# Kernel tuning notes

Measured on AMD Instinct MI355X. Metric: run time of the kernel, lower is better.

## Reference

```python
import jax, jax.numpy as jnp
import numpy as np

EPS = 1e-5

def _ln(x, g, b):
    mu = x.mean(-1, keepdims=True)
    v = x.var(-1, keepdims=True)
    return g * (x - mu) / jnp.sqrt(v + EPS) + b

def _mlp(x, W0, b0, g0, be0, W1, b1, g1, be1, W2, b2, nm):
    # Linear -> LN -> GELU, Linear -> LN -> GELU, Linear -> split into complex
    h = jax.nn.gelu(_ln(x @ W0 + b0, g0, be0), approximate=False)
    h = jax.nn.gelu(_ln(h @ W1 + b1, g1, be1), approximate=False)
    o = h @ W2 + b2
    return jax.lax.complex(o[..., :nm], o[..., nm:])

def _forward(x, w_W0, w_b0, w_g0, w_be0, w_W1, w_b1, w_g1, w_be1, w_W2, w_b2,
             h_W0, h_b0, h_g0, h_be0, h_W1, h_b1, h_g1, h_be1, h_W2, h_b2,
             freq_r, freq_i, mixer_w, mixer_b, norm_g, norm_b, sc_w, sc_b):
    B, C, H, W = x.shape
    m1, m2 = freq_r.shape[2], freq_r.shape[3]
    wc = jnp.linspace(0.0, 1.0, W, dtype=x.dtype)
    hc = jnp.linspace(0.0, 1.0, H, dtype=x.dtype)
    # W-basis conditioned on values and normalized w-coordinate
    x_nhwc = x.transpose(0, 2, 3, 1)                                   # (B,H,W,C)
    w_in = jnp.concatenate([x_nhwc, jnp.broadcast_to(wc[None, None, :, None], (B, H, W, 1))], -1)
    wb = _mlp(w_in, w_W0, w_b0, w_g0, w_be0, w_W1, w_b1, w_g1, w_be1, w_W2, w_b2, m2)  # (B,H,W,m2) c64
    xc = x.astype(jnp.complex64)
    t = jnp.einsum('bchw,bhwm->bchm', xc, wb)                          # (B,C,H,m2)
    # H-basis conditioned on real part of W-transformed signal
    h_in = jnp.concatenate([t.real.transpose(0, 3, 2, 1),
                            jnp.broadcast_to(hc[None, None, :, None], (B, m2, H, 1))], -1)
    hb = _mlp(h_in, h_W0, h_b0, h_g0, h_be0, h_W1, h_b1, h_g1, h_be1, h_W2, h_b2, m1)  # (B,m2,H,m1)
    t2 = jnp.einsum('bchm,bmhn->bcnm', t, hb)                          # (B,C,m1,m2)
    Wf = jax.lax.complex(freq_r, freq_i)                               # (C,O,m1,m2)
    proc = jnp.einsum('bixy,oixy->boxy', t2, Wf)                       # (B,O,m1,m2)
    # Inverse transforms via conjugate-transposed bases
    rec_h = jnp.einsum('bonm,bmhn->bohm', proc, jnp.conj(hb))          # (B,O,H,m2)
    rec = jnp.einsum('bohm,bhwm->bohw', rec_h, jnp.conj(wb))           # (B,O,H,W)
    y = rec.real / (H * W)
    y = jnp.einsum('bchw,oc->bohw', y, mixer_w) + mixer_b[None, :, None, None]
    mu = y.mean(1, keepdims=True)
    v = y.var(1, keepdims=True)
    y = norm_g[None, :, None, None] * (y - mu) / jnp.sqrt(v + EPS) + norm_b[None, :, None, None]
    y = jax.nn.gelu(y, approximate=False)
    sc = jnp.einsum('bchw,oc->bohw', x, sc_w) + sc_b[None, :, None, None]
    return jax.nn.gelu(y + sc, approximate=False)

def setup_inputs() -> dict:
    key = jax.random.key(0)
    B, C, O, H, W, M1, M2, HD = 8, 64, 64, 192, 192, 48, 48, 64
    ks = jax.random.split(key, 12)
    r = lambda k, sh, s=0.05: jax.random.normal(k, sh, jnp.float32) * s
    d = dict(x=jax.random.normal(ks[0], (B, C, H, W), jnp.float32))
    d.update(w_W0=r(ks[1], (C + 1, HD)), w_b0=jnp.zeros(HD), w_g0=jnp.ones(HD), w_be0=jnp.zeros(HD),
             w_W1=r(ks[2], (HD, HD)), w_b1=jnp.zeros(HD), w_g1=jnp.ones(HD), w_be1=jnp.zeros(HD),
             w_W2=r(ks[3], (HD, 2 * M2)), w_b2=jnp.zeros(2 * M2))
    d.update(h_W0=r(ks[4], (C + 1, HD)), h_b0=jnp.zeros(HD), h_g0=jnp.ones(HD), h_be0=jnp.zeros(HD),
             h_W1=r(ks[5], (HD, HD)), h_b1=jnp.zeros(HD), h_g1=jnp.ones(HD), h_be1=jnp.zeros(HD),
             h_W2=r(ks[6], (HD, 2 * M1)), h_b2=jnp.zeros(2 * M1))
    d.update(freq_r=r(ks[7], (C, O, M1, M2), 0.1), freq_i=r(ks[8], (C, O, M1, M2), 0.1),
             mixer_w=r(ks[9], (O, O)), mixer_b=jnp.zeros(O),
             norm_g=jnp.ones(O), norm_b=jnp.zeros(O),
             sc_w=r(ks[10], (O, C)), sc_b=jnp.zeros(O))
    return d

def reference(x, w_W0, w_b0, w_g0, w_be0, w_W1, w_b1, w_g1, w_be1, w_W2, w_b2,
              h_W0, h_b0, h_g0, h_be0, h_W1, h_b1, h_g1, h_be1, h_W2, h_b2,
              freq_r, freq_i, mixer_w, mixer_b, norm_g, norm_b, sc_w, sc_b):
    return _forward(x, w_W0, w_b0, w_g0, w_be0, w_W1, w_b1, w_g1, w_be1, w_W2, w_b2,
                    h_W0, h_b0, h_g0, h_be0, h_W1, h_b1, h_g1, h_be1, h_W2, h_b2,
                    freq_r, freq_i, mixer_w, mixer_b, norm_g, norm_b, sc_w, sc_b)
```

## Files before the change

### kernel.cpp

```cpp
#include <hip/hip_runtime.h>
#include <math.h>

#define LN_EPS 1e-5f

typedef short bf16x8 __attribute__((ext_vector_type(8)));
typedef float f32x4  __attribute__((ext_vector_type(4)));

__device__ __forceinline__ float gelu_f(float v) {
    return 0.5f * v * (1.0f + erff(v * 0.70710678118654752f));
}
__device__ __forceinline__ unsigned short f2bf(float f) {
    __bf16 h = (__bf16)f;
    unsigned short u;
    __builtin_memcpy(&u, &h, 2);
    return u;
}
__device__ __forceinline__ float bf2f(unsigned short h) {
    return __uint_as_float(((unsigned)h) << 16);
}

__global__ __launch_bounds__(256) void k0_swizzle(
    const float* __restrict__ wW0, const float* __restrict__ wW1, const float* __restrict__ wW2,
    const float* __restrict__ hW0, const float* __restrict__ hW1, const float* __restrict__ hW2,
    uint4* __restrict__ dst)
// ... 205 lines not shown
    for (int cc = 0; cc < 16; ++cc) {
        int c = cc*4 + quad;
        float v = x[((b*64 + c)*192 + h)*192 + (w0 + r)];
        unsigned short hv = f2bf(v);
        aHi[r*72 + c] = hv;
        aLo[r*72 + c] = f2bf(v - bf2f(hv));
    }
    mlp_body(aHi, aLo, wsw, W0full + 64*64, b0, g0, be0, b1, g1, be1, b2,
             (float)w0, wb_r, wb_i, bh*192 + w0);
}

__global__ __launch_bounds__(256) void k3_mlp_h(
    const float* __restrict__ t_r, const float* __restrict__ W0full,
    const float* __restrict__ b0, const float* __restrict__ g0, const float* __restrict__ be0,
    const float* __restrict__ b1, const float* __restrict__ g1, const float* __restrict__ be1,
    const float* __restrict__ b2,
    const uint4* __restrict__ wsw,
    float* __restrict__ hb_r, float* __restrict__ hb_i)
{
    __shared__ unsigned short aHi[64*72];
    __shared__ unsigned short aLo[64*72];
    int tid = threadIdx.x;
    int wv = __builtin_amdgcn_readfirstlane(tid >> 6);
    int lane = tid & 63, li = lane & 15, quad = lane >> 4;
    int hq = blockIdx.x % 3;
    int bm = blockIdx.x / 3;
    int b = bm / 48, m = bm % 48;
    int h0 = hq * 64;
    int r = wv*16 + li;
    {
        const float4* tb = (const float4*)(t_r + ((b*48 + m)*192 + h0 + r)*64);
        #pragma unroll
        for (int q = 0; q < 4; ++q) {
            float4 v4 = tb[quad*4 + q];
            float vv[4] = {v4.x, v4.y, v4.z, v4.w};
            int k0 = quad*16 + q*4;
            #pragma unroll
            for (int e = 0; e < 4; ++e) {
                unsigned short hv = f2bf(vv[e]);
                aHi[r*72 + k0 + e] = hv;
                aLo[r*72 + k0 + e] = f2bf(vv[e] - bf2f(hv));
            }
        }
    }
    mlp_body(aHi, aLo, wsw, W0full + 64*64, b0, g0, be0, b1, g1, be1, b2,
             (float)h0, hb_r, hb_i, bm*192 + h0);
}

__global__ __launch_bounds__(256) void k2_t(
    const float* __restrict__ x,
    const float* __restrict__ wb_r, const float* __restrict__ wb_i,
    float* __restrict__ t_r, float* __restrict__ t_i)
{
    __shared__ unsigned short aHi[64*72];
    __shared__ unsigned short aLo[64*72];
    __shared__ uint4 bfrag[1536];
    float* cbuf = (float*)bfrag;
    int bh = blockIdx.x;
    int b = bh / 192, h = bh % 192;
    int tid = threadIdx.x;
    int wv = __builtin_amdgcn_readfirstlane(tid >> 6);
    int lane = tid & 63, li = lane & 15, quad = lane >> 4;
    int rbase = wv*16;
    int row = rbase + li;

    f32x4 acc[6];
    {
        f32x4 z = {0.f, 0.f, 0.f, 0.f};
        #pragma unroll
        for (int nt = 0; nt < 6; ++nt) acc[nt] = z;
    }
    union U { uint4 u; bf16x8 b8; };

    for (int w0 = 0; w0 < 192; w0 += 64) {
        if (w0) __syncthreads();
        {
            const float4* srow = (const float4*)(x + ((b*64 + row)*192 + h)*192 + w0) + quad*4;
            #pragma unroll
            for (int q = 0; q < 4; ++q) {
                float4 v4 = srow[q];
                float vv[4] = {v4.x, v4.y, v4.z, v4.w};
                int k0 = quad*16 + q*4;
                #pragma unroll
                for (int e = 0; e < 4; ++e) {
                    unsigned short hv = f2bf(vv[e]);
                    aHi[row*72 + k0 + e] = hv;
                    aLo[row*72 + k0 + e] = f2bf(vv[e] - bf2f(hv));
                }
            }
        }
        for (int t = tid >> 6; t < 12; t += 4) {
            int nt = t >> 1, ks = t & 1;
            const float* src = (nt < 3) ? wb_r : wb_i;
            int col = (nt < 3 ? nt : nt - 3)*16 + li;
            const float* sp = src + (bh*192 + w0 + ks*32 + quad*8)*48 + col;
            unsigned hi8[8], lo8[8];
            #pragma unroll
            for (int j = 0; j < 8; ++j) {
                float v = sp[j*48];
                unsigned short hv = f2bf(v);
                hi8[j] = hv;
                lo8[j] = f2bf(v - bf2f(hv));
            }
            uint4 ph, pl;
            ph.x = hi8[0] | (hi8[1]<<16); ph.y = hi8[2] | (hi8[3]<<16);
            ph.z = hi8[4] | (hi8[5]<<16); ph.w = hi8[6] | (hi8[7]<<16);
            pl.x = lo8[0] | (lo8[1]<<16); pl.y = lo8[2] | (lo8[3]<<16);
            pl.z = lo8[4] | (lo8[5]<<16); pl.w = lo8[6] | (lo8[7]<<16);
            bfrag[t*64 + lane]       = ph;
            bfrag[768 + t*64 + lane] = pl;
        }
        __syncthreads();
        bf16x8 aH[2], aL[2];
        #pragma unroll
        for (int ks = 0; ks < 2; ++ks) {
            aH[ks] = *(const bf16x8*)&aHi[row*72 + ks*32 + quad*8];
            aL[ks] = *(const bf16x8*)&aLo[row*72 + ks*32 + quad*8];
        }
        #pragma unroll
        for (int nt = 0; nt < 6; ++nt) {
            f32x4 a = acc[nt];
            #pragma unroll
            for (int ks = 0; ks < 2; ++ks) {
                int t = nt*2 + ks;
                U bh_, bl_;
                bh_.u = bfrag[t*64 + lane];
                bl_.u = bfrag[768 + t*64 + lane];
                a = __builtin_amdgcn_mfma_f32_16x16x32_bf16(aH[ks], bh_.b8, a, 0, 0, 0);
                a = __builtin_amdgcn_mfma_f32_16x16x32_bf16(aH[ks], bl_.b8, a, 0, 0, 0);
                a = __builtin_amdgcn_mfma_f32_16x16x32_bf16(aL[ks], bh_.b8, a, 0, 0, 0);
            }
            acc[nt] = a;
        }
    }
    __syncthreads();
    #pragma unroll
    for (int nt = 0; nt < 3; ++nt) {
        int m = nt*16 + li;
        #pragma unroll
        for (int rg = 0; rg < 4; ++rg) {
            int c = rbase + quad*4 + rg;
            cbuf[m*67 + c] = acc[nt][rg];
        }
    }
    __syncthreads();
    for (int idx = tid; idx < 3072; idx += 256) {
        int m = idx >> 6, c = idx & 63;
        t_r[((b*48 + m)*192 + h)*64 + c] = cbuf[m*67 + c];
    }
    __syncthreads();
    #pragma unroll
    for (int nt = 3; nt < 6; ++nt) {
        int m = (nt - 3)*16 + li;
        #pragma unroll
        for (int rg = 0; rg < 4; ++rg) {
            int c = rbase + quad*4 + rg;
            cbuf[m*67 + c] = acc[nt][rg];
        }
    }
    __syncthreads();
    for (int idx = tid; idx < 3072; idx += 256) {
        int m = idx >> 6, c = idx & 63;
        t_i[((b*48 + m)*192 + h)*64 + c] = cbuf[m*67 + c];
    }
}

__global__ __launch_bounds__(256) void k4_t2(
    const float* __restrict__ t_r, const float* __restrict__ t_i,
    const float* __restrict__ hb_r, const float* __restrict__ hb_i,
    float* __restrict__ t2_r, float* __restrict__ t2_i)
{
    __shared__ unsigned short aHi[64*72];
    __shared__ unsigned short aLo[64*72];
    __shared__ uint4 bfrag[1536];
    int bm = blockIdx.x;
    int b = bm / 48, m = bm % 48;
    int tid = threadIdx.x;
    int wv = __builtin_amdgcn_readfirstlane(tid >> 6);
    int lane = tid & 63, li = lane & 15, quad = lane >> 4;
    int rbase = wv*16;
    int row = rbase + li;

    f32x4 acc[6];
    {
        f32x4 z = {0.f, 0.f, 0.f, 0.f};
// ... 31 lines not shown
            }
            const float* sp = src + (bm*192 + h0 + ks*32 + quad*8)*48 + col;
            unsigned hi8[8], lo8[8];
            #pragma unroll
            for (int j = 0; j < 8; ++j) {
                float v = sgn * sp[j*48];
                unsigned short hv = f2bf(v);
                hi8[j] = hv;
                lo8[j] = f2bf(v - bf2f(hv));
            }
            uint4 ph, pl;
            ph.x = hi8[0] | (hi8[1]<<16); ph.y = hi8[2] | (hi8[3]<<16);
            ph.z = hi8[4] | (hi8[5]<<16); ph.w = hi8[6] | (hi8[7]<<16);
            pl.x = lo8[0] | (lo8[1]<<16); pl.y = lo8[2] | (lo8[3]<<16);
            pl.z = lo8[4] | (lo8[5]<<16); pl.w = lo8[6] | (lo8[7]<<16);
            bfrag[t*64 + lane]       = ph;
            bfrag[768 + t*64 + lane] = pl;
        }
        __syncthreads();
        bf16x8 aH[2], aL[2];
        #pragma unroll
        for (int ks = 0; ks < 2; ++ks) {
            aH[ks] = *(const bf16x8*)&aHi[row*72 + ks*32 + quad*8];
            aL[ks] = *(const bf16x8*)&aLo[row*72 + ks*32 + quad*8];
        }
        #pragma unroll
        for (int nt = 0; nt < 6; ++nt) {
            f32x4 a = acc[nt];
            #pragma unroll
            for (int ks = 0; ks < 2; ++ks) {
                int t = nt*2 + ks;
                U bh_, bl_;
                bh_.u = bfrag[t*64 + lane];
                bl_.u = bfrag[768 + t*64 + lane];
                a = __builtin_amdgcn_mfma_f32_16x16x32_bf16(aH[ks], bh_.b8, a, 0, 0, 0);
                a = __builtin_amdgcn_mfma_f32_16x16x32_bf16(aH[ks], bl_.b8, a, 0, 0, 0);
                a = __builtin_amdgcn_mfma_f32_16x16x32_bf16(aL[ks], bh_.b8, a, 0, 0, 0);
            }
            acc[nt] = a;
        }
    }
    #pragma unroll
    for (int nt = 0; nt < 6; ++nt) {
        #pragma unroll
        for (int rg = 0; rg < 4; ++rg) {
            int c = rbase + quad*4 + rg;
            float v = acc[nt][rg];
            if (nt < 3) t2_r[((b*64 + c)*48 + nt*16 + li)*48 + m]       = v;
            else        t2_i[((b*64 + c)*48 + (nt - 3)*16 + li)*48 + m] = v;
        }
    }
}

__global__ __launch_bounds__(256) void k5_proc(
    const float* __restrict__ t2_r, const float* __restrict__ t2_i,
    const float* __restrict__ fr, const float* __restrict__ fi,
    float* __restrict__ proc_r, float* __restrict__ proc_i)
{
    int og = blockIdx.x & 31;
    int ch = blockIdx.x >> 5;
    int nm = ch*256 + threadIdx.x;
    int n = nm / 48, mm = nm % 48;
    int o0 = og*2;
    float p0r[8], p0i[8], p1r[8], p1i[8];
    #pragma unroll
    for (int bb = 0; bb < 8; ++bb) { p0r[bb]=0.f; p0i[bb]=0.f; p1r[bb]=0.f; p1i[bb]=0.f; }
    for (int i = 0; i < 64; ++i) {
        float w0r = fr[(o0*64 + i)*2304 + nm];
        float w0i = fi[(o0*64 + i)*2304 + nm];
        float w1r = fr[((o0+1)*64 + i)*2304 + nm];
        float w1i = fi[((o0+1)*64 + i)*2304 + nm];
        #pragma unroll
        for (int bb = 0; bb < 8; ++bb) {
            float tr = t2_r[(bb*64 + i)*2304 + nm];
            float ti = t2_i[(bb*64 + i)*2304 + nm];
            p0r[bb] = fmaf(tr, w0r, fmaf(-ti, w0i, p0r[bb]));
            p0i[bb] = fmaf(tr, w0i, fmaf( ti, w0r, p0i[bb]));
            p1r[bb] = fmaf(tr, w1r, fmaf(-ti, w1i, p1r[bb]));
            p1i[bb] = fmaf(tr, w1i, fmaf( ti, w1r, p1i[bb]));
        }
    }
    #pragma unroll
    for (int bb = 0; bb < 8; ++bb) {
        int base0 = ((bb*48 + mm)*64 + o0)*48 + n;
        proc_r[base0]      = p0r[bb];
        proc_i[base0]      = p0i[bb];
        proc_r[base0 + 48] = p1r[bb];
        proc_i[base0 + 48] = p1i[bb];
    }
}

__global__ __launch_bounds__(256) void k6_rech(
    const float* __restrict__ proc_r, const float* __restrict__ proc_i,
    const float* __restrict__ hb_r, const float* __restrict__ hb_i,
    float* __restrict__ rh_r, float* __restrict__ rh_i)
{
    __shared__ unsigned short aHi[64*104];
    __shared__ unsigned short aLo[64*104];
    __shared__ uint4 bfrag[1536];
    int hq = blockIdx.x % 3;
    int bm = blockIdx.x / 3;
    int b = bm / 48, m = bm % 48;
    int h0 = hq * 64;
    int tid = threadIdx.x;
    int wv = __builtin_amdgcn_readfirstlane(tid >> 6);
    int lane = tid & 63, li = lane & 15, quad = lane >> 4;
    int rbase = wv*16;
    int row = rbase + li;

    {
        int hr = bm*192 + h0 + row;
        const float4* pr = (const float4*)(hb_r + hr*48) + quad*3;
        const float4* pi = (const float4*)(hb_i + hr*48) + quad*3;
        #pragma unroll
        for (int q = 0; q < 3; ++q) {
            float4 vr = pr[q];
            float4 vi = pi[q];
            int k0 = quad*12 + q*4;
            float vs[8] = {vr.x, vr.y, vr.z, vr.w, vi.x, vi.y, vi.z, vi.w};
            #pragma unroll
            for (int e = 0; e < 4; ++e) {
                unsigned short h1 = f2bf(vs[e]);
                aHi[row*104 + k0 + e] = h1;
                aLo[row*104 + k0 + e] = f2bf(vs[e] - bf2f(h1));
                unsigned short h2 = f2bf(vs[4+e]);
                aHi[row*104 + 48 + k0 + e] = h2;
                aLo[row*104 + 48 + k0 + e] = f2bf(vs[4+e] - bf2f(h2));
            }
        }
    }
    union U { uint4 u; bf16x8 b8; };
    bf16x8 aH[3], aL[3];
    #pragma unroll
    for (int ks = 0; ks < 3; ++ks) {
        aH[ks] = *(const bf16x8*)&aHi[row*104 + ks*32 + quad*8];
        aL[ks] = *(const bf16x8*)&aLo[row*104 + ks*32 + quad*8];
    }

    f32x4 accR[4], accI[4];
    for (int pass = 0; pass < 2; ++pass) {
        if (pass) __syncthreads();
        for (int t = tid >> 6; t < 12; t += 4) {
            int ks = t % 3;
            int nt = t / 3;
            int o = nt*16 + li;
            int kk0 = ks*32 + quad*8;
            const float* srcp;
            int n0;
            float sgn;
            if (kk0 < 48) { srcp = pass ? proc_i : proc_r; n0 = kk0;      sgn = 1.f; }
            else          { srcp = pass ? proc_r : proc_i; n0 = kk0 - 48; sgn = pass ? -1.f : 1.f; }
            const float* sp = srcp + ((b*48 + m)*64 + o)*48 + n0;
            float4 f0 = *(const float4*)sp;
            float4 f1 = *(const float4*)(sp + 4);
            float vv[8] = {f0.x, f0.y, f0.z, f0.w, f1.x, f1.y, f1.z, f1.w};
            unsigned hi8[8], lo8[8];
            #pragma unroll
            for (int j = 0; j < 8; ++j) {
                float v = sgn * vv[j];
                unsigned short hv = f2bf(v);
                hi8[j] = hv;
                lo8[j] = f2bf(v - bf2f(hv));
            }
            uint4 ph, pl;
            ph.x = hi8[0] | (hi8[1]<<16); ph.y = hi8[2] | (hi8[3]<<16);
            ph.z = hi8[4] | (hi8[5]<<16); ph.w = hi8[6] | (hi8[7]<<16);
            pl.x = lo8[0] | (lo8[1]<<16); pl.y = lo8[2] | (lo8[3]<<16);
            pl.z = lo8[4] | (lo8[5]<<16); pl.w = lo8[6] | (lo8[7]<<16);
            bfrag[t*64 + lane]       = ph;
            bfrag[768 + t*64 + lane] = pl;
        }
        __syncthreads();
        f32x4* acc = pass ? accI : accR;
        #pragma unroll
        for (int nt = 0; nt < 4; ++nt) {
            f32x4 a = {0.f, 0.f, 0.f, 0.f};
            #pragma unroll
            for (int ks = 0; ks < 3; ++ks) {
                int t = nt*3 + ks;
                U bh_, bl_;
                bh_.u = bfrag[t*64 + lane];
                bl_.u = bfrag[768 + t*64 + lane];
                a = __builtin_amdgcn_mfma_f32_16x16x32_bf16(aH[ks], bh_.b8, a, 0, 0, 0);
                a = __builtin_amdgcn_mfma_f32_16x16x32_bf16(aH[ks], bl_.b8, a, 0, 0, 0);
                a = __builtin_amdgcn_mfma_f32_16x16x32_bf16(aL[ks], bh_.b8, a, 0, 0, 0);
            }
            acc[nt] = a;
        }
    }
    #pragma unroll
    for (int nt = 0; nt < 4; ++nt) {
        int o = nt*16 + li;
        #pragma unroll
        for (int rg = 0; rg < 4; ++rg) {
            int hrow = h0 + rbase + quad*4 + rg;
            int a = (bm*192 + hrow)*64 + o;
            rh_r[a] = accR[nt][rg];
            rh_i[a] = accI[nt][rg];
        }
    }
}

__global__ __launch_bounds__(256) void k7_rec(
    const float* __restrict__ rh_r, const float* __restrict__ rh_i,
    const float* __restrict__ wb_r, const float* __restrict__ wb_i,
    const float* __restrict__ x,
    const uint4* __restrict__ msw,
    const float* __restrict__ mb,
    const float* __restrict__ nrm_g, const float* __restrict__ nrm_b,
    const float* __restrict__ sb,
    float* __restrict__ out)
{
    __shared__ unsigned short aHi[64*104];
    __shared__ unsigned short aLo[64*104];
    __shared__ uint4 bfrag[1536];
    float* cbuf = (float*)bfrag;

    int wq = blockIdx.x % 3;
    int bh = blockIdx.x / 3;
    int b = bh / 192, h = bh % 192;
    int w0 = wq * 64;
    int tid = threadIdx.x;
    int wv = __builtin_amdgcn_readfirstlane(tid >> 6);
    int lane = tid & 63, li = lane & 15, quad = lane >> 4;
    int rbase = wv*16;
    int row = rbase + li;

    {
        int pix = bh*192 + w0 + row;
        const float4* pr = (const float4*)(wb_r + pix*48) + quad*3;
        const float4* pi = (const float4*)(wb_i + pix*48) + quad*3;
        #pragma unroll
        for (int q = 0; q < 3; ++q) {
            float4 vr = pr[q];
            float4 vi = pi[q];
            int k0 = quad*12 + q*4;
            float vs[8] = {vr.x, vr.y, vr.z, vr.w, vi.x, vi.y, vi.z, vi.w};
            #pragma unroll
            for (int e = 0; e < 4; ++e) {
                unsigned short h1 = f2bf(vs[e]);
                aHi[row*104 + k0 + e] = h1;
                aLo[row*104 + k0 + e] = f2bf(vs[e] - bf2f(h1));
                unsigned short h2 = f2bf(vs[4+e]);
                aHi[row*104 + 48 + k0 + e] = h2;
                aLo[row*104 + 48 + k0 + e] = f2bf(vs[4+e] - bf2f(h2));
            }
        }
    }
    for (int t = tid >> 6; t < 12; t += 4) {
        int ks = t % 3;
        int nt = t / 3;
        int o = nt*16 + li;
        unsigned hi8[8], lo8[8];
        #pragma unroll
        for (int j = 0; j < 8; ++j) {
            int kk = ks*32 + quad*8 + j;
            const float* src = (kk < 48) ? rh_r : rh_i;
            int m = (kk < 48) ? kk : kk - 48;
            float v = src[((b*48 + m)*192 + h)*64 + o];
            unsigned short hv = f2bf(v);
            hi8[j] = hv;
            lo8[j] = f2bf(v - bf2f(hv));
        }
        uint4 ph, pl;
        ph.x = hi8[0] | (hi8[1]<<16); ph.y = hi8[2] | (hi8[3]<<16);
        ph.z = hi8[4] | (hi8[5]<<16); ph.w = hi8[6] | (hi8[7]<<16);
        pl.x = lo8[0] | (lo8[1]<<16); pl.y = lo8[2] | (lo8[3]<<16);
        pl.z = lo8[4] | (lo8[5]<<16); pl.w = lo8[6] | (lo8[7]<<16);
        bfrag[t*64 + lane]       = ph;
        bfrag[768 + t*64 + lane] = pl;
    }
    __syncthreads();

    union U { uint4 u; bf16x8 b; };
    bf16x8 aH[3], aL[3];
    #pragma unroll
    for (int ks = 0; ks < 3; ++ks) {
        aH[ks] = *(const bf16x8*)&aHi[row*104 + ks*32 + quad*8];
        aL[ks] = *(const bf16x8*)&aLo[row*104 + ks*32 + quad*8];
    }
    f32x4 acc[4];
    #pragma unroll
    for (int nt = 0; nt < 4; ++nt) {
        f32x4 a = {0.f, 0.f, 0.f, 0.f};
        #pragma unroll
        for (int ks = 0; ks < 3; ++ks) {
            int t = nt*3 + ks;
            U bh_, bl_;
            bh_.u = bfrag[t*64 + lane];
            bl_.u = bfrag[768 + t*64 + lane];
            a = __builtin_amdgcn_mfma_f32_16x16x32_bf16(aH[ks], bh_.b, a, 0, 0, 0);
            a = __builtin_amdgcn_mfma_f32_16x16x32_bf16(aH[ks], bl_.b, a, 0, 0, 0);
            a = __builtin_amdgcn_mfma_f32_16x16x32_bf16(aL[ks], bh_.b, a, 0, 0, 0);
        }
        acc[nt] = a;
    }

    const float s = 1.0f / 36864.0f;
    #pragma unroll
    for (int nt = 0; nt < 4; ++nt) {
        int o = nt*16 + li;
        #pragma unroll
        for (int rg = 0; rg < 4; ++rg) {
            int prow = rbase + quad*4 + rg;
            float v = acc[nt][rg] * s;
            unsigned short hv = f2bf(v);
            aHi[prow*104 + o] = hv;
            aLo[prow*104 + o] = f2bf(v - bf2f(hv));
        }
    }
    f32x4 accy[4];
    gemm64s<4, 104>(aHi, aLo, msw, 0, row, quad, lane, accy);

    float vals[4][4];
    float s1[4] = {0,0,0,0}, s2[4] = {0,0,0,0};
    #pragma unroll
    for (int nt = 0; nt < 4; ++nt) {
        int o = nt*16 + li;
        float bv = mb[o];
        #pragma unroll
        for (int rg = 0; rg < 4; ++rg) {
            float v = accy[nt][rg] + bv;
            vals[nt][rg] = v;
            s1[rg] += v;
            s2[rg] = fmaf(v, v, s2[rg]);
        }
    }
    #pragma unroll
    for (int d = 1; d < 16; d <<= 1) {
        #pragma unroll
        for (int rg = 0; rg < 4; ++rg) {
            s1[rg] += __shfl_xor(s1[rg], d, 64);
            s2[rg] += __shfl_xor(s2[rg], d, 64);
        }
    }

    #pragma unroll
    for (int cc = 0; cc < 16; ++cc) {
        int c = cc*4 + quad;
        float v = x[((b*64 + c)*192 + h)*192 + w0 + row];
        unsigned short hv = f2bf(v);
        aHi[row*104 + c] = hv;
        aLo[row*104 + c] = f2bf(v - bf2f(hv));
    }
    gemm64s<4, 104>(aHi, aLo, msw, 8, row, quad, lane, acc);

    __syncthreads();
    #pragma unroll
    for (int nt = 0; nt < 4; ++nt) {
        int o = nt*16 + li;
        float gv = nrm_g[o], bev = nrm_b[o], sbv = sb[o];
        #pragma unroll
        for (int rg = 0; rg < 4; ++rg) {
            float mu   = s1[rg] * 0.015625f;
            float rstd = rsqrtf(s2[rg]*0.015625f - mu*mu + LN_EPS);
            float v  = gelu_f(fmaf((vals[nt][rg] - mu)*rstd, gv, bev));
            float sc = acc[nt][rg] + sbv;
            int prow = rbase + quad*4 + rg;
            cbuf[prow*67 + o] = gelu_f(v + sc);
        }
    }
    __syncthreads();
    #pragma unroll
    for (int it = 0; it < 16; ++it) {
        int o = it*4 + (tid >> 6);
        int pix = tid & 63;
        out[((b*64 + o)*192 + h)*192 + w0 + pix] = cbuf[pix*67 + o];
    }
}

extern "C" void kernel_launch(void* const* d_in, const int* in_sizes, int n_in,
                              void* d_out, int out_size, void* d_ws, size_t ws_size,
                              hipStream_t stream)
{
    (void)in_sizes; (void)n_in; (void)out_size; (void)ws_size;
    const float* x    = (const float*)d_in[0];
    const float* wW0  = (const float*)d_in[1];
    const float* wb0  = (const float*)d_in[2];
    const float* wg0  = (const float*)d_in[3];
    const float* wbe0 = (const float*)d_in[4];
    const float* wW1  = (const float*)d_in[5];
    const float* wb1  = (const float*)d_in[6];
    const float* wg1  = (const float*)d_in[7];
    const float* wbe1 = (const float*)d_in[8];
    const float* wW2  = (const float*)d_in[9];
    const float* wb2  = (const float*)d_in[10];
    const float* hW0  = (const float*)d_in[11];
    const float* hb0  = (const float*)d_in[12];
    const float* hg0  = (const float*)d_in[13];
    const float* hbe0 = (const float*)d_in[14];
    const float* hW1  = (const float*)d_in[15];
    const float* hb1  = (const float*)d_in[16];
    const float* hg1  = (const float*)d_in[17];
    const float* hbe1 = (const float*)d_in[18];
    const float* hW2  = (const float*)d_in[19];
    const float* hb2  = (const float*)d_in[20];
    const float* fr   = (const float*)d_in[21];
    const float* fi   = (const float*)d_in[22];
    const float* mw   = (const float*)d_in[23];
    const float* mb   = (const float*)d_in[24];
    const float* ngp  = (const float*)d_in[25];
    const float* nbp  = (const float*)d_in[26];
    const float* sw   = (const float*)d_in[27];
    const float* sb   = (const float*)d_in[28];
    float* out = (float*)d_out;

    float* ws   = (float*)d_ws;
    float* wbr  = ws;
    float* wbi  = ws + 14155776;
    float* t_r  = ws + 28311552;
    float* t_i  = ws + 33030144;
    float* hbr  = ws + 37748736;
    float* hbi  = ws + 41287680;
    float* t2r  = ws + 44826624;
    float* t2i  = ws + 46006272;
    float* prr  = ws + 47185920;
    float* pri  = ws + 48365568;
    float* rhr  = t_r;
    float* rhi  = t_i;
    float* wswb = ws + 49545216;
    uint4* wsw  = (uint4*)wswb;
    uint4* msw  = (uint4*)t2r;

    k0_swizzle<<<dim3(6), dim3(256), 0, stream>>>(wW0, wW1, wW2, hW0, hW1, hW2, wsw);
    k1_mlp_w<<<dim3(4608), dim3(256), 0, stream>>>(x, wW0, wb0, wg0, wbe0,
                                                   wb1, wg1, wbe1, wb2, wsw, wbr, wbi);
    k2_t<<<dim3(1536), dim3(256), 0, stream>>>(x, wbr, wbi, t_r, t_i);
    k3_mlp_h<<<dim3(1152), dim3(256), 0, stream>>>(t_r, hW0, hb0, hg0, hbe0,
                                                   hb1, hg1, hbe1, hb2, wsw + 3584, hbr, hbi);
    k4_t2<<<dim3(384), dim3(256), 0, stream>>>(t_r, t_i, hbr, hbi, t2r, t2i);
    k5_proc<<<dim3(288), dim3(256), 0, stream>>>(t2r, t2i, fr, fi, prr, pri);
    k0b_swizzle<<<dim3(2), dim3(256), 0, stream>>>(mw, sw, msw);
    k6_rech<<<dim3(1152), dim3(256), 0, stream>>>(prr, pri, hbr, hbi, rhr, rhi);
    k7_rec<<<dim3(4608), dim3(256), 0, stream>>>(rhr, rhi, wbr, wbi,
                                                 x, msw, mb, ngp, nbp, sb, out);
}
```

Measured before the change: 573.8 us.

## Halve B-fragment LDS staging in k2/k6/k7 and shrink k5 blocks

In k2_t, k6_rech and k7_rec, the B-fragment staging buffer is cut in half by loading and consuming the N tiles in two rounds. The smaller LDS footprint, with aliased shared-memory layouts, is meant to let more blocks fit on each CU. k5_proc now uses 64-thread blocks with four times as many blocks, to spread its small grid across more CUs. In exchange, the three MFMA kernels gain extra __syncthreads barriers and serialize fragment loading against compute.

```diff
diff --git a/kernel.cpp b/kernel.cpp
--- a/kernel.cpp
+++ b/kernel.cpp
@@ -281,10 +281,13 @@
     const float* __restrict__ wb_r, const float* __restrict__ wb_i,
     float* __restrict__ t_r, float* __restrict__ t_i)
 {
-    __shared__ unsigned short aHi[64*72];
-    __shared__ unsigned short aLo[64*72];
-    __shared__ uint4 bfrag[1536];
-    float* cbuf = (float*)bfrag;
+    __shared__ unsigned long long smem_u[30720/8];
+    unsigned char* smem = (unsigned char*)smem_u;
+    unsigned short* aHi = (unsigned short*)smem;
+    unsigned short* aLo = (unsigned short*)(smem + 9216);
+    uint4* bfrag = (uint4*)(smem + 18432);
+    float* cbuf  = (float*)smem;
+
     int bh = blockIdx.x;
     int b = bh / 192, h = bh % 192;
     int tid = threadIdx.x;
@@ -302,7 +305,6 @@
     union U { uint4 u; bf16x8 b8; };
 
     for (int w0 = 0; w0 < 192; w0 += 64) {
-        if (w0) __syncthreads();
         {
             const float4* srow = (const float4*)(x + ((b*64 + row)*192 + h)*192 + w0) + quad*4;
             #pragma unroll
@@ -318,28 +320,6 @@
                 }
             }
         }
-        for (int t = tid >> 6; t < 12; t += 4) {
-            int nt = t >> 1, ks = t & 1;
-            const float* src = (nt < 3) ? wb_r : wb_i;
-            int col = (nt < 3 ? nt : nt - 3)*16 + li;
-            const float* sp = src + (bh*192 + w0 + ks*32 + quad*8)*48 + col;
-            unsigned hi8[8], lo8[8];
-            #pragma unroll
-            for (int j = 0; j < 8; ++j) {
-                float v = sp[j*48];
-                unsigned short hv = f2bf(v);
-                hi8[j] = hv;
-                lo8[j] = f2bf(v - bf2f(hv));
-            }
-            uint4 ph, pl;
-            ph.x = hi8[0] | (hi8[1]<<16); ph.y = hi8[2] | (hi8[3]<<16);
-            ph.z = hi8[4] | (hi8[5]<<16); ph.w = hi8[6] | (hi8[7]<<16);
-            pl.x = lo8[0] | (lo8[1]<<16); pl.y = lo8[2] | (lo8[3]<<16);
-            pl.z = lo8[4] | (lo8[5]<<16); pl.w = lo8[6] | (lo8[7]<<16);
-            bfrag[t*64 + lane]       = ph;
-            bfrag[768 + t*64 + lane] = pl;
-        }
-        __syncthreads();
         bf16x8 aH[2], aL[2];
         #pragma unroll
         for (int ks = 0; ks < 2; ++ks) {
@@ -347,19 +327,46 @@
             aL[ks] = *(const bf16x8*)&aLo[row*72 + ks*32 + quad*8];
         }
         #pragma unroll
-        for (int nt = 0; nt < 6; ++nt) {
-            f32x4 a = acc[nt];
-            #pragma unroll
-            for (int ks = 0; ks < 2; ++ks) {
-                int t = nt*2 + ks;
-                U bh_, bl_;
-                bh_.u = bfrag[t*64 + lane];
-                bl_.u = bfrag[768 + t*64 + lane];
-                a = __builtin_amdgcn_mfma_f32_16x16x32_bf16(aH[ks], bh_.b8, a, 0, 0, 0);
-                a = __builtin_amdgcn_mfma_f32_16x16x32_bf16(aH[ks], bl_.b8, a, 0, 0, 0);
-                a = __builtin_amdgcn_mfma_f32_16x16x32_bf16(aL[ks], bh_.b8, a, 0, 0, 0);
-            }
-            acc[nt] = a;
+        for (int rb = 0; rb < 2; ++rb) {
+            if (w0 || rb) __syncthreads();
+            for (int t = 6*rb + wv; t < 6*rb + 6; t += 4) {
+                int nt = t >> 1, ks = t & 1;
+                const float* src = (nt < 3) ? wb_r : wb_i;
+                int col = (nt < 3 ? nt : nt - 3)*16 + li;
+                const float* sp = src + (bh*192 + w0 + ks*32 + quad*8)*48 + col;
+                unsigned hi8[8], lo8[8];
+                #pragma unroll
+                for (int j = 0; j < 8; ++j) {
+                    float v = sp[j*48];
+                    unsigned short hv = f2bf(v);
+                    hi8[j] = hv;
+                    lo8[j] = f2bf(v - bf2f(hv));
+                }
+                uint4 ph, pl;
+                ph.x = hi8[0] | (hi8[1]<<16); ph.y = hi8[2] | (hi8[3]<<16);
+                ph.z = hi8[4] | (hi8[5]<<16); ph.w = hi8[6] | (hi8[7]<<16);
+                pl.x = lo8[0] | (lo8[1]<<16); pl.y = lo8[2] | (lo8[3]<<16);
+                pl.z = lo8[4] | (lo8[5]<<16); pl.w = lo8[6] | (lo8[7]<<16);
+                int slot = t - 6*rb;
+                bfrag[slot*64 + lane]       = ph;
+                bfrag[384 + slot*64 + lane] = pl;
+            }
+            __syncthreads();
+            #pragma unroll
+            for (int nt = 3*rb; nt < 3*rb + 3; ++nt) {
+                f32x4 a = acc[nt];
+                #pragma unroll
+                for (int ks = 0; ks < 2; ++ks) {
+                    int slot = nt*2 + ks - 6*rb;
+                    U bh_, bl_;
+                    bh_.u = bfrag[slot*64 + lane];
+                    bl_.u = bfrag[384 + slot*64 + lane];
+                    a = __builtin_amdgcn_mfma_f32_16x16x32_bf16(aH[ks], bh_.b8, a, 0, 0, 0);
+                    a = __builtin_amdgcn_mfma_f32_16x16x32_bf16(aH[ks], bl_.b8, a, 0, 0, 0);
+                    a = __builtin_amdgcn_mfma_f32_16x16x32_bf16(aL[ks], bh_.b8, a, 0, 0, 0);
+                }
+                acc[nt] = a;
+            }
         }
     }
     __syncthreads();
@@ -497,14 +504,14 @@
     }
 }
 
-__global__ __launch_bounds__(256) void k5_proc(
+__global__ __launch_bounds__(64) void k5_proc(
     const float* __restrict__ t2_r, const float* __restrict__ t2_i,
     const float* __restrict__ fr, const float* __restrict__ fi,
     float* __restrict__ proc_r, float* __restrict__ proc_i)
 {
     int og = blockIdx.x & 31;
     int ch = blockIdx.x >> 5;
-    int nm = ch*256 + threadIdx.x;
+    int nm = ch*64 + threadIdx.x;
     int n = nm / 48, mm = nm % 48;
     int o0 = og*2;
     float p0r[8], p0i[8], p1r[8], p1i[8];
@@ -540,9 +547,12 @@
     const float* __restrict__ hb_r, const float* __restrict__ hb_i,
     float* __restrict__ rh_r, float* __restrict__ rh_i)
 {
-    __shared__ unsigned short aHi[64*104];
-    __shared__ unsigned short aLo[64*104];
-    __shared__ uint4 bfrag[1536];
+    __shared__ unsigned long long smem_u[38912/8];
+    unsigned char* smem = (unsigned char*)smem_u;
+    unsigned short* aHi = (unsigned short*)smem;
+    unsigned short* aLo = (unsigned short*)(smem + 13312);
+    uint4* bfrag = (uint4*)(smem + 26624);
+
     int hq = blockIdx.x % 3;
     int bm = blockIdx.x / 3;
     int b = bm / 48, m = bm % 48;
@@ -583,54 +593,59 @@
     }
 
     f32x4 accR[4], accI[4];
+    #pragma unroll
     for (int pass = 0; pass < 2; ++pass) {
-        if (pass) __syncthreads();
-        for (int t = tid >> 6; t < 12; t += 4) {
-            int ks = t % 3;
-            int nt = t / 3;
-            int o = nt*16 + li;
-            int kk0 = ks*32 + quad*8;
-            const float* srcp;
-            int n0;
-            float sgn;
-            if (kk0 < 48) { srcp = pass ? proc_i : proc_r; n0 = kk0;      sgn = 1.f; }
-            else          { srcp = pass ? proc_r : proc_i; n0 = kk0 - 48; sgn = pass ? -1.f : 1.f; }
-            const float* sp = srcp + ((b*48 + m)*64 + o)*48 + n0;
-            float4 f0 = *(const float4*)sp;
-            float4 f1 = *(const float4*)(sp + 4);
-            float vv[8] = {f0.x, f0.y, f0.z, f0.w, f1.x, f1.y, f1.z, f1.w};
-            unsigned hi8[8], lo8[8];
-            #pragma unroll
-            for (int j = 0; j < 8; ++j) {
-                float v = sgn * vv[j];
-                unsigned short hv = f2bf(v);
-                hi8[j] = hv;
-                lo8[j] = f2bf(v - bf2f(hv));
-            }
-            uint4 ph, pl;
-            ph.x = hi8[0] | (hi8[1]<<16); ph.y = hi8[2] | (hi8[3]<<16);
-            ph.z = hi8[4] | (hi8[5]<<16); ph.w = hi8[6] | (hi8[7]<<16);
-            pl.x = lo8[0] | (lo8[1]<<16); pl.y = lo8[2] | (lo8[3]<<16);
-            pl.z = lo8[4] | (lo8[5]<<16); pl.w = lo8[6] | (lo8[7]<<16);
-            bfrag[t*64 + lane]       = ph;
-            bfrag[768 + t*64 + lane] = pl;
-        }
-        __syncthreads();
         f32x4* acc = pass ? accI : accR;
         #pragma unroll
-        for (int nt = 0; nt < 4; ++nt) {
-            f32x4 a = {0.f, 0.f, 0.f, 0.f};
-            #pragma unroll
-            for (int ks = 0; ks < 3; ++ks) {
-                int t = nt*3 + ks;
-                U bh_, bl_;
-                bh_.u = bfrag[t*64 + lane];
-                bl_.u = bfrag[768 + t*64 + lane];
-                a = __builtin_amdgcn_mfma_f32_16x16x32_bf16(aH[ks], bh_.b8, a, 0, 0, 0);
-                a = __builtin_amdgcn_mfma_f32_16x16x32_bf16(aH[ks], bl_.b8, a, 0, 0, 0);
-                a = __builtin_amdgcn_mfma_f32_16x16x32_bf16(aL[ks], bh_.b8, a, 0, 0, 0);
-            }
-            acc[nt] = a;
+        for (int rb = 0; rb < 2; ++rb) {
+            if (pass || rb) __syncthreads();
+            for (int t = 6*rb + wv; t < 6*rb + 6; t += 4) {
+                int ks = t % 3;
+                int nt = t / 3;
+                int o = nt*16 + li;
+                int kk0 = ks*32 + quad*8;
+                const float* srcp;
+                int n0;
+                float sgn;
+                if (kk0 < 48) { srcp = pass ? proc_i : proc_r; n0 = kk0;      sgn = 1.f; }
+                else          { srcp = pass ? proc_r : proc_i; n0 = kk0 - 48; sgn = pass ? -1.f : 1.f; }
+                const float* sp = srcp + ((b*48 + m)*64 + o)*48 + n0;
+                float4 f0 = *(const float4*)sp;
+                float4 f1 = *(const float4*)(sp + 4);
+                float vv[8] = {f0.x, f0.y, f0.z, f0.w, f1.x, f1.y, f1.z, f1.w};
+                unsigned hi8[8], lo8[8];
+                #pragma unroll
+                for (int j = 0; j < 8; ++j) {
+                    float v = sgn * vv[j];
+                    unsigned short hv = f2bf(v);
+                    hi8[j] = hv;
+                    lo8[j] = f2bf(v - bf2f(hv));
+                }
+                uint4 ph, pl;
+                ph.x = hi8[0] | (hi8[1]<<16); ph.y = hi8[2] | (hi8[3]<<16);
+                ph.z = hi8[4] | (hi8[5]<<16); ph.w = hi8[6] | (hi8[7]<<16);
+                pl.x = lo8[0] | (lo8[1]<<16); pl.y = lo8[2] | (lo8[3]<<16);
+                pl.z = lo8[4] | (lo8[5]<<16); pl.w = lo8[6] | (lo8[7]<<16);
+                int slot = t - 6*rb;
+                bfrag[slot*64 + lane]       = ph;
+                bfrag[384 + slot*64 + lane] = pl;
+            }
+            __syncthreads();
+            #pragma unroll
+            for (int nt = 2*rb; nt < 2*rb + 2; ++nt) {
+                f32x4 a = {0.f, 0.f, 0.f, 0.f};
+                #pragma unroll
+                for (int ks = 0; ks < 3; ++ks) {
+                    int slot = nt*3 + ks - 6*rb;
+                    U bh_, bl_;
+                    bh_.u = bfrag[slot*64 + lane];
+                    bl_.u = bfrag[384 + slot*64 + lane];
+                    a = __builtin_amdgcn_mfma_f32_16x16x32_bf16(aH[ks], bh_.b8, a, 0, 0, 0);
+                    a = __builtin_amdgcn_mfma_f32_16x16x32_bf16(aH[ks], bl_.b8, a, 0, 0, 0);
+                    a = __builtin_amdgcn_mfma_f32_16x16x32_bf16(aL[ks], bh_.b8, a, 0, 0, 0);
+                }
+                acc[nt] = a;
+            }
         }
     }
     #pragma unroll
@@ -656,10 +671,12 @@
     const float* __restrict__ sb,
     float* __restrict__ out)
 {
-    __shared__ unsigned short aHi[64*104];
-    __shared__ unsigned short aLo[64*104];
-    __shared__ uint4 bfrag[1536];
-    float* cbuf = (float*)bfrag;
+    __shared__ unsigned long long smem_u[38912/8];
+    unsigned char* smem = (unsigned char*)smem_u;
+    unsigned short* aHi = (unsigned short*)smem;
+    unsigned short* aLo = (unsigned short*)(smem + 13312);
+    uint4* bfrag = (uint4*)(smem + 26624);
+    float* cbuf  = (float*)smem;
 
     int wq = blockIdx.x % 3;
     int bh = blockIdx.x / 3;
@@ -692,31 +709,6 @@
             }
         }
     }
-    for (int t = tid >> 6; t < 12; t += 4) {
-        int ks = t % 3;
-        int nt = t / 3;
-        int o = nt*16 + li;
-        unsigned hi8[8], lo8[8];
-        #pragma unroll
-        for (int j = 0; j < 8; ++j) {
-            int kk = ks*32 + quad*8 + j;
-            const float* src = (kk < 48) ? rh_r : rh_i;
-            int m = (kk < 48) ? kk : kk - 48;
-            float v = src[((b*48 + m)*192 + h)*64 + o];
-            unsigned short hv = f2bf(v);
-            hi8[j] = hv;
-            lo8[j] = f2bf(v - bf2f(hv));
-        }
-        uint4 ph, pl;
-        ph.x = hi8[0] | (hi8[1]<<16); ph.y = hi8[2] | (hi8[3]<<16);
-        ph.z = hi8[4] | (hi8[5]<<16); ph.w = hi8[6] | (hi8[7]<<16);
-        pl.x = lo8[0] | (lo8[1]<<16); pl.y = lo8[2] | (lo8[3]<<16);
-        pl.z = lo8[4] | (lo8[5]<<16); pl.w = lo8[6] | (lo8[7]<<16);
-        bfrag[t*64 + lane]       = ph;
-        bfrag[768 + t*64 + lane] = pl;
-    }
-    __syncthreads();
-
     union U { uint4 u; bf16x8 b; };
     bf16x8 aH[3], aL[3];
     #pragma unroll
@@ -724,21 +716,51 @@
         aH[ks] = *(const bf16x8*)&aHi[row*104 + ks*32 + quad*8];
         aL[ks] = *(const bf16x8*)&aLo[row*104 + ks*32 + quad*8];
     }
+
     f32x4 acc[4];
     #pragma unroll
-    for (int nt = 0; nt < 4; ++nt) {
-        f32x4 a = {0.f, 0.f, 0.f, 0.f};
-        #pragma unroll
-        for (int ks = 0; ks < 3; ++ks) {
-            int t = nt*3 + ks;
-            U bh_, bl_;
-            bh_.u = bfrag[t*64 + lane];
-            bl_.u = bfrag[768 + t*64 + lane];
-            a = __builtin_amdgcn_mfma_f32_16x16x32_bf16(aH[ks], bh_.b, a, 0, 0, 0);
-            a = __builtin_amdgcn_mfma_f32_16x16x32_bf16(aH[ks], bl_.b, a, 0, 0, 0);
-            a = __builtin_amdgcn_mfma_f32_16x16x32_bf16(aL[ks], bh_.b, a, 0, 0, 0);
-        }
-        acc[nt] = a;
+    for (int rb = 0; rb < 2; ++rb) {
+        if (rb) __syncthreads();
+        for (int t = 6*rb + wv; t < 6*rb + 6; t += 4) {
+            int ks = t % 3;
+            int nt = t / 3;
+            int o = nt*16 + li;
+            unsigned hi8[8], lo8[8];
+            #pragma unroll
+            for (int j = 0; j < 8; ++j) {
+                int kk = ks*32 + quad*8 + j;
+                const float* src = (kk < 48) ? rh_r : rh_i;
+                int m = (kk < 48) ? kk : kk - 48;
+                float v = src[((b*48 + m)*192 + h)*64 + o];
+                unsigned short hv = f2bf(v);
+                hi8[j] = hv;
+                lo8[j] = f2bf(v - bf2f(hv));
+            }
+            uint4 ph, pl;
+            ph.x = hi8[0] | (hi8[1]<<16); ph.y = hi8[2] | (hi8[3]<<16);
+            ph.z = hi8[4] | (hi8[5]<<16); ph.w = hi8[6] | (hi8[7]<<16);
+            pl.x = lo8[0] | (lo8[1]<<16); pl.y = lo8[2] | (lo8[3]<<16);
+            pl.z = lo8[4] | (lo8[5]<<16); pl.w = lo8[6] | (lo8[7]<<16);
+            int slot = t - 6*rb;
+            bfrag[slot*64 + lane]       = ph;
+            bfrag[384 + slot*64 + lane] = pl;
+        }
+        __syncthreads();
+        #pragma unroll
+        for (int nt = 2*rb; nt < 2*rb + 2; ++nt) {
+            f32x4 a = {0.f, 0.f, 0.f, 0.f};
+            #pragma unroll
+            for (int ks = 0; ks < 3; ++ks) {
+                int slot = nt*3 + ks - 6*rb;
+                U bh_, bl_;
+                bh_.u = bfrag[slot*64 + lane];
+                bl_.u = bfrag[384 + slot*64 + lane];
+                a = __builtin_amdgcn_mfma_f32_16x16x32_bf16(aH[ks], bh_.b, a, 0, 0, 0);
+                a = __builtin_amdgcn_mfma_f32_16x16x32_bf16(aH[ks], bl_.b, a, 0, 0, 0);
+                a = __builtin_amdgcn_mfma_f32_16x16x32_bf16(aL[ks], bh_.b, a, 0, 0, 0);
+            }
+            acc[nt] = a;
+        }
     }
 
     const float s = 1.0f / 36864.0f;
@@ -874,7 +896,7 @@
     k3_mlp_h<<<dim3(1152), dim3(256), 0, stream>>>(t_r, hW0, hb0, hg0, hbe0,
                                                    hb1, hg1, hbe1, hb2, wsw + 3584, hbr, hbi);
     k4_t2<<<dim3(384), dim3(256), 0, stream>>>(t_r, t_i, hbr, hbi, t2r, t2i);
-    k5_proc<<<dim3(288), dim3(256), 0, stream>>>(t2r, t2i, fr, fi, prr, pri);
+    k5_proc<<<dim3(1152), dim3(64), 0, stream>>>(t2r, t2i, fr, fi, prr, pri);
     k0b_swizzle<<<dim3(2), dim3(256), 0, stream>>>(mw, sw, msw);
     k6_rech<<<dim3(1152), dim3(256), 0, stream>>>(prr, pri, hbr, hbi, rhr, rhi);
     k7_rec<<<dim3(4608), dim3(256), 0, stream>>>(rhr, rhi, wbr, wbi,
```

Measured after the change: 577.4 us. Within noise of the previous version (+0.6%).

## Reuse rec_h fragments across W tiles in k7 and widen k5 output blocking

Applied to the files above, without the earlier changes.

k7_rec now handles a whole H row per block, looping over three 64-pixel W tiles. The rec_h B-fragments are converted and staged into shared memory once and reused by all three tiles, instead of being rebuilt by three separate blocks. k5_proc computes four output channels per thread with 64-thread blocks, so each t2 load feeds more FMAs. In exchange there are fewer, longer blocks (1536 instead of 4608 for k7, and 576 blocks of 64 threads for k5), which lowers parallelism and occupancy. The msw weight buffer moves to its own workspace slot so its swizzle kernel can run first.

```diff
diff --git a/kernel.cpp b/kernel.cpp
--- a/kernel.cpp
+++ b/kernel.cpp
@@ -497,41 +497,47 @@
     }
 }
 
-__global__ __launch_bounds__(256) void k5_proc(
+__global__ __launch_bounds__(64) void k5_proc(
     const float* __restrict__ t2_r, const float* __restrict__ t2_i,
     const float* __restrict__ fr, const float* __restrict__ fi,
     float* __restrict__ proc_r, float* __restrict__ proc_i)
 {
-    int og = blockIdx.x & 31;
-    int ch = blockIdx.x >> 5;
-    int nm = ch*256 + threadIdx.x;
+    int og = blockIdx.x & 15;
+    int ch = blockIdx.x >> 4;
+    int nm = ch*64 + threadIdx.x;
     int n = nm / 48, mm = nm % 48;
-    int o0 = og*2;
-    float p0r[8], p0i[8], p1r[8], p1i[8];
-    #pragma unroll
-    for (int bb = 0; bb < 8; ++bb) { p0r[bb]=0.f; p0i[bb]=0.f; p1r[bb]=0.f; p1i[bb]=0.f; }
+    int o0 = og*4;
+    float pr[4][8], pi[4][8];
+    #pragma unroll
+    for (int q = 0; q < 4; ++q)
+        #pragma unroll
+        for (int bb = 0; bb < 8; ++bb) { pr[q][bb] = 0.f; pi[q][bb] = 0.f; }
     for (int i = 0; i < 64; ++i) {
-        float w0r = fr[(o0*64 + i)*2304 + nm];
-        float w0i = fi[(o0*64 + i)*2304 + nm];
-        float w1r = fr[((o0+1)*64 + i)*2304 + nm];
-        float w1i = fi[((o0+1)*64 + i)*2304 + nm];
+        float wr[4], wi[4];
+        #pragma unroll
+        for (int q = 0; q < 4; ++q) {
+            wr[q] = fr[((o0 + q)*64 + i)*2304 + nm];
+            wi[q] = fi[((o0 + q)*64 + i)*2304 + nm];
+        }
         #pragma unroll
         for (int bb = 0; bb < 8; ++bb) {
             float tr = t2_r[(bb*64 + i)*2304 + nm];
             float ti = t2_i[(bb*64 + i)*2304 + nm];
-            p0r[bb] = fmaf(tr, w0r, fmaf(-ti, w0i, p0r[bb]));
-            p0i[bb] = fmaf(tr, w0i, fmaf( ti, w0r, p0i[bb]));
-            p1r[bb] = fmaf(tr, w1r, fmaf(-ti, w1i, p1r[bb]));
-            p1i[bb] = fmaf(tr, w1i, fmaf( ti, w1r, p1i[bb]));
+            #pragma unroll
+            for (int q = 0; q < 4; ++q) {
+                pr[q][bb] = fmaf(tr, wr[q], fmaf(-ti, wi[q], pr[q][bb]));
+                pi[q][bb] = fmaf(tr, wi[q], fmaf( ti, wr[q], pi[q][bb]));
+            }
         }
     }
     #pragma unroll
     for (int bb = 0; bb < 8; ++bb) {
         int base0 = ((bb*48 + mm)*64 + o0)*48 + n;
-        proc_r[base0]      = p0r[bb];
-        proc_i[base0]      = p0i[bb];
-        proc_r[base0 + 48] = p1r[bb];
-        proc_i[base0 + 48] = p1i[bb];
+        #pragma unroll
+        for (int q = 0; q < 4; ++q) {
+            proc_r[base0 + q*48] = pr[q][bb];
+            proc_i[base0 + q*48] = pi[q][bb];
+        }
     }
 }
 
@@ -659,39 +665,16 @@
     __shared__ unsigned short aHi[64*104];
     __shared__ unsigned short aLo[64*104];
     __shared__ uint4 bfrag[1536];
-    float* cbuf = (float*)bfrag;
-
-    int wq = blockIdx.x % 3;
-    int bh = blockIdx.x / 3;
+    float* cbuf = (float*)aHi;
+
+    int bh = blockIdx.x;
     int b = bh / 192, h = bh % 192;
-    int w0 = wq * 64;
     int tid = threadIdx.x;
     int wv = __builtin_amdgcn_readfirstlane(tid >> 6);
     int lane = tid & 63, li = lane & 15, quad = lane >> 4;
     int rbase = wv*16;
     int row = rbase + li;
 
-    {
-        int pix = bh*192 + w0 + row;
-        const float4* pr = (const float4*)(wb_r + pix*48) + quad*3;
-        const float4* pi = (const float4*)(wb_i + pix*48) + quad*3;
-        #pragma unroll
-        for (int q = 0; q < 3; ++q) {
-            float4 vr = pr[q];
-            float4 vi = pi[q];
-            int k0 = quad*12 + q*4;
-            float vs[8] = {vr.x, vr.y, vr.z, vr.w, vi.x, vi.y, vi.z, vi.w};
-            #pragma unroll
-            for (int e = 0; e < 4; ++e) {
-                unsigned short h1 = f2bf(vs[e]);
-                aHi[row*104 + k0 + e] = h1;
-                aLo[row*104 + k0 + e] = f2bf(vs[e] - bf2f(h1));
-                unsigned short h2 = f2bf(vs[4+e]);
-                aHi[row*104 + 48 + k0 + e] = h2;
-                aLo[row*104 + 48 + k0 + e] = f2bf(vs[4+e] - bf2f(h2));
-            }
-        }
-    }
     for (int t = tid >> 6; t < 12; t += 4) {
         int ks = t % 3;
         int nt = t / 3;
@@ -718,99 +701,125 @@
     __syncthreads();
 
     union U { uint4 u; bf16x8 b; };
-    bf16x8 aH[3], aL[3];
-    #pragma unroll
-    for (int ks = 0; ks < 3; ++ks) {
-        aH[ks] = *(const bf16x8*)&aHi[row*104 + ks*32 + quad*8];
-        aL[ks] = *(const bf16x8*)&aLo[row*104 + ks*32 + quad*8];
-    }
-    f32x4 acc[4];
-    #pragma unroll
-    for (int nt = 0; nt < 4; ++nt) {
-        f32x4 a = {0.f, 0.f, 0.f, 0.f};
+    for (int wq = 0; wq < 3; ++wq) {
+        int w0 = wq * 64;
+
+        {
+            int pix = bh*192 + w0 + row;
+            const float4* pr = (const float4*)(wb_r + pix*48) + quad*3;
+            const float4* pi = (const float4*)(wb_i + pix*48) + quad*3;
+            #pragma unroll
+            for (int q = 0; q < 3; ++q) {
+                float4 vr = pr[q];
+                float4 vi = pi[q];
+                int k0 = quad*12 + q*4;
+                float vs[8] = {vr.x, vr.y, vr.z, vr.w, vi.x, vi.y, vi.z, vi.w};
+                #pragma unroll
+                for (int e = 0; e < 4; ++e) {
+                    unsigned short h1 = f2bf(vs[e]);
+                    aHi[row*104 + k0 + e] = h1;
+                    aLo[row*104 + k0 + e] = f2bf(vs[e] - bf2f(h1));
+                    unsigned short h2 = f2bf(vs[4+e]);
+                    aHi[row*104 + 48 + k0 + e] = h2;
+                    aLo[row*104 + 48 + k0 + e] = f2bf(vs[4+e] - bf2f(h2));
+                }
+            }
+        }
+        bf16x8 aH[3], aL[3];
         #pragma unroll
         for (int ks = 0; ks < 3; ++ks) {
-            int t = nt*3 + ks;
-            U bh_, bl_;
-            bh_.u = bfrag[t*64 + lane];
-            bl_.u = bfrag[768 + t*64 + lane];
-            a = __builtin_amdgcn_mfma_f32_16x16x32_bf16(aH[ks], bh_.b, a, 0, 0, 0);
-            a = __builtin_amdgcn_mfma_f32_16x16x32_bf16(aH[ks], bl_.b, a, 0, 0, 0);
-            a = __builtin_amdgcn_mfma_f32_16x16x32_bf16(aL[ks], bh_.b, a, 0, 0, 0);
-        }
-        acc[nt] = a;
-    }
-
-    const float s = 1.0f / 36864.0f;
-    #pragma unroll
-    for (int nt = 0; nt < 4; ++nt) {
-        int o = nt*16 + li;
-        #pragma unroll
-        for (int rg = 0; rg < 4; ++rg) {
-            int prow = rbase + quad*4 + rg;
-            float v = acc[nt][rg] * s;
+            aH[ks] = *(const bf16x8*)&aHi[row*104 + ks*32 + quad*8];
+            aL[ks] = *(const bf16x8*)&aLo[row*104 + ks*32 + quad*8];
+        }
+        f32x4 acc[4];
+        #pragma unroll
+        for (int nt = 0; nt < 4; ++nt) {
+            f32x4 a = {0.f, 0.f, 0.f, 0.f};
+            #pragma unroll
+            for (int ks = 0; ks < 3; ++ks) {
+                int t = nt*3 + ks;
+                U bh_, bl_;
+                bh_.u = bfrag[t*64 + lane];
+                bl_.u = bfrag[768 + t*64 + lane];
+                a = __builtin_amdgcn_mfma_f32_16x16x32_bf16(aH[ks], bh_.b, a, 0, 0, 0);
+                a = __builtin_amdgcn_mfma_f32_16x16x32_bf16(aH[ks], bl_.b, a, 0, 0, 0);
+                a = __builtin_amdgcn_mfma_f32_16x16x32_bf16(aL[ks], bh_.b, a, 0, 0, 0);
+            }
+            acc[nt] = a;
+        }
+
+        const float s = 1.0f / 36864.0f;
+        #pragma unroll
+        for (int nt = 0; nt < 4; ++nt) {
+            int o = nt*16 + li;
+            #pragma unroll
+            for (int rg = 0; rg < 4; ++rg) {
+                int prow = rbase + quad*4 + rg;
+                float v = acc[nt][rg] * s;
+                unsigned short hv = f2bf(v);
+                aHi[prow*104 + o] = hv;
+                aLo[prow*104 + o] = f2bf(v - bf2f(hv));
+            }
+        }
+        f32x4 accy[4];
+        gemm64s<4, 104>(aHi, aLo, msw, 0, row, quad, lane, accy);
+
+        float vals[4][4];
+        float s1[4] = {0,0,0,0}, s2[4] = {0,0,0,0};
+        #pragma unroll
+        for (int nt = 0; nt < 4; ++nt) {
+            int o = nt*16 + li;
+            float bv = mb[o];
+            #pragma unroll
+            for (int rg = 0; rg < 4; ++rg) {
+                float v = accy[nt][rg] + bv;
+                vals[nt][rg] = v;
+                s1[rg] += v;
+                s2[rg] = fmaf(v, v, s2[rg]);
+            }
+        }
+        #pragma unroll
+        for (int d = 1; d < 16; d <<= 1) {
+            #pragma unroll
+            for (int rg = 0; rg < 4; ++rg) {
+                s1[rg] += __shfl_xor(s1[rg], d, 64);
+                s2[rg] += __shfl_xor(s2[rg], d, 64);
+            }
+        }
+
+        #pragma unroll
+        for (int cc = 0; cc < 16; ++cc) {
+            int c = cc*4 + quad;
+            float v = x[((b*64 + c)*192 + h)*192 + w0 + row];
             unsigned short hv = f2bf(v);
-            aHi[prow*104 + o] = hv;
-            aLo[prow*104 + o] = f2bf(v - bf2f(hv));
-        }
-    }
-    f32x4 accy[4];
-    gemm64s<4, 104>(aHi, aLo, msw, 0, row, quad, lane, accy);
-
-    float vals[4][4];
-    float s1[4] = {0,0,0,0}, s2[4] = {0,0,0,0};
-    #pragma unroll
-    for (int nt = 0; nt < 4; ++nt) {
-        int o = nt*16 + li;
-        float bv = mb[o];
-        #pragma unroll
-        for (int rg = 0; rg < 4; ++rg) {
-            float v = accy[nt][rg] + bv;
-            vals[nt][rg] = v;
-            s1[rg] += v;
-            s2[rg] = fmaf(v, v, s2[rg]);
-        }
-    }
-    #pragma unroll
-    for (int d = 1; d < 16; d <<= 1) {
-        #pragma unroll
-        for (int rg = 0; rg < 4; ++rg) {
-            s1[rg] += __shfl_xor(s1[rg], d, 64);
-            s2[rg] += __shfl_xor(s2[rg], d, 64);
-        }
-    }
-
-    #pragma unroll
-    for (int cc = 0; cc < 16; ++cc) {
-        int c = cc*4 + quad;
-        float v = x[((b*64 + c)*192 + h)*192 + w0 + row];
-        unsigned short hv = f2bf(v);
-        aHi[row*104 + c] = hv;
-        aLo[row*104 + c] = f2bf(v - bf2f(hv));
-    }
-    gemm64s<4, 104>(aHi, aLo, msw, 8, row, quad, lane, acc);
-
-    __syncthreads();
-    #pragma unroll
-    for (int nt = 0; nt < 4; ++nt) {
-        int o = nt*16 + li;
-        float gv = nrm_g[o], bev = nrm_b[o], sbv = sb[o];
-        #pragma unroll
-        for (int rg = 0; rg < 4; ++rg) {
-            float mu   = s1[rg] * 0.015625f;
-            float rstd = rsqrtf(s2[rg]*0.015625f - mu*mu + LN_EPS);
-            float v  = gelu_f(fmaf((vals[nt][rg] - mu)*rstd, gv, bev));
-            float sc = acc[nt][rg] + sbv;
-            int prow = rbase + quad*4 + rg;
-            cbuf[prow*67 + o] = gelu_f(v + sc);
-        }
-    }
-    __syncthreads();
-    #pragma unroll
-    for (int it = 0; it < 16; ++it) {
-        int o = it*4 + (tid >> 6);
-        int pix = tid & 63;
-        out[((b*64 + o)*192 + h)*192 + w0 + pix] = cbuf[pix*67 + o];
+            aHi[row*104 + c] = hv;
+            aLo[row*104 + c] = f2bf(v - bf2f(hv));
+        }
+        gemm64s<4, 104>(aHi, aLo, msw, 8, row, quad, lane, acc);
+
+        __syncthreads();
+        #pragma unroll
+        for (int nt = 0; nt < 4; ++nt) {
+            int o = nt*16 + li;
+            float gv = nrm_g[o], bev = nrm_b[o], sbv = sb[o];
+            #pragma unroll
+            for (int rg = 0; rg < 4; ++rg) {
+                float mu   = s1[rg] * 0.015625f;
+                float rstd = rsqrtf(s2[rg]*0.015625f - mu*mu + LN_EPS);
+                float v  = gelu_f(fmaf((vals[nt][rg] - mu)*rstd, gv, bev));
+                float sc = acc[nt][rg] + sbv;
+                int prow = rbase + quad*4 + rg;
+                cbuf[prow*67 + o] = gelu_f(v + sc);
+            }
+        }
+        __syncthreads();
+        #pragma unroll
+        for (int it = 0; it < 16; ++it) {
+            int o = it*4 + (tid >> 6);
+            int pix = tid & 63;
+            out[((b*64 + o)*192 + h)*192 + w0 + pix] = cbuf[pix*67 + o];
+        }
+        __syncthreads();
     }
 }
 
@@ -865,18 +874,18 @@
     float* rhi  = t_i;
     float* wswb = ws + 49545216;
     uint4* wsw  = (uint4*)wswb;
-    uint4* msw  = (uint4*)t2r;
+    uint4* msw  = (uint4*)(ws + 49545216 + 32768);
 
     k0_swizzle<<<dim3(6), dim3(256), 0, stream>>>(wW0, wW1, wW2, hW0, hW1, hW2, wsw);
+    k0b_swizzle<<<dim3(2), dim3(256), 0, stream>>>(mw, sw, msw);
     k1_mlp_w<<<dim3(4608), dim3(256), 0, stream>>>(x, wW0, wb0, wg0, wbe0,
                                                    wb1, wg1, wbe1, wb2, wsw, wbr, wbi);
     k2_t<<<dim3(1536), dim3(256), 0, stream>>>(x, wbr, wbi, t_r, t_i);
     k3_mlp_h<<<dim3(1152), dim3(256), 0, stream>>>(t_r, hW0, hb0, hg0, hbe0,
                                                    hb1, hg1, hbe1, hb2, wsw + 3584, hbr, hbi);
     k4_t2<<<dim3(384), dim3(256), 0, stream>>>(t_r, t_i, hbr, hbi, t2r, t2i);
-    k5_proc<<<dim3(288), dim3(256), 0, stream>>>(t2r, t2i, fr, fi, prr, pri);
-    k0b_swizzle<<<dim3(2), dim3(256), 0, stream>>>(mw, sw, msw);
+    k5_proc<<<dim3(576), dim3(64), 0, stream>>>(t2r, t2i, fr, fi, prr, pri);
     k6_rech<<<dim3(1152), dim3(256), 0, stream>>>(prr, pri, hbr, hbi, rhr, rhi);
-    k7_rec<<<dim3(4608), dim3(256), 0, stream>>>(rhr, rhi, wbr, wbi,
+    k7_rec<<<dim3(1536), dim3(256), 0, stream>>>(rhr, rhi, wbr, wbi,
                                                  x, msw, mb, ngp, nbp, sb, out);
 }
```

After: 682.4 us. 18.9% more time.
